# Kernel tuning notes

Measured on AMD Instinct MI355X. Metric: run time of the kernel, lower is better.

The kernel has to match this reference:

```python
import jax, jax.numpy as jnp
import numpy as np

DIM = 1024
HEADS = 16
SEQ_H = 32
SEQ_W = 32
HEAD_DIM = DIM // HEADS          # 64
ROT_DIM = HEAD_DIM // 4          # 16 per axis (lucidrains RotaryEmbedding dim)
FULL_ROT = 2 * ROT_DIM           # 32 channels rotated (axial: H-axis + W-axis)


def axial_freqs():
    # lucidrains 'pixel' mode: freqs = linspace(1, max_freq/2, dim//2) * pi, pos = linspace(-1, 1, steps)
    max_freq = SEQ_H * SEQ_W
    base = jnp.linspace(1.0, max_freq / 2.0, ROT_DIM // 2) * jnp.pi  # (rot//2,)
    th = jnp.linspace(-1.0, 1.0, SEQ_H)[:, None] * base[None, :]     # (H, rot//2)
    tw = jnp.linspace(-1.0, 1.0, SEQ_W)[:, None] * base[None, :]     # (W, rot//2)
    fh = jnp.repeat(th, 2, axis=-1)                                   # (H, rot)
    fw = jnpp_repeat = jnp.repeat(tw, 2, axis=-1)                     # (W, rot)
    fh = jnp.broadcast_to(fh[:, None, :], (SEQ_H, SEQ_W, ROT_DIM))
    fw = jnp.broadcast_to(fw[None, :, :], (SEQ_H, SEQ_W, ROT_DIM))
    return jnp.concatenate([fh, fw], axis=-1)                         # (H, W, FULL_ROT)


def rotate_half(t):
    # '... (d r) -> ... d r' with r=2, then (-x2, x1) interleaved back
    x = t.reshape(t.shape[:-1] + (t.shape[-1] // 2, 2))
    x1, x2 = x[..., 0], x[..., 1]
    return jnp.stack([-x2, x1], axis=-1).reshape(t.shape)


def apply_rope(t, cos, sin):
    # t: (B, heads, H, W, head_dim); only first FULL_ROT channels are rotated
    t_rot, t_pass = t[..., :FULL_ROT], t[..., FULL_ROT:]
    t_rot = t_rot * cos + rotate_half(t_rot) * sin
    return jnp.concatenate([t_rot, t_pass], axis=-1)


def setup_inputs() -> dict:
    key = jax.random.key(0)
    k1, k2, k3 = jax.random.split(key, 3)
    B, N = 8, SEQ_H * SEQ_W
    x = jax.random.normal(k1, (B, N, DIM), dtype=jnp.float32)
    Wqkv = jax.random.normal(k2, (3 * DIM, DIM), dtype=jnp.float32) * 0.02
    Wproj = jax.random.normal(k3, (DIM, DIM), dtype=jnp.float32) * 0.02
    bproj = jnp.zeros((DIM,), dtype=jnp.float32)
    return {"x": x, "Wqkv": Wqkv, "Wproj": Wproj, "bproj": bproj}


def reference(x, Wqkv, Wproj, bproj):
    B, N, C = x.shape
    qkv = jnp.einsum('bnc,fc->bnf', x, Wqkv)          # (B, N, 3C)
    q, k, v = jnp.split(qkv, 3, axis=-1)

    def to_grid(t):  # (B, N, C) -> (B, heads, H, W, hd)
        return t.reshape(B, SEQ_H, SEQ_W, HEADS, HEAD_DIM).transpose(0, 3, 1, 2, 4)

    q, k, v = to_grid(q), to_grid(k), to_grid(v)
    freqs = axial_freqs()
    cos, sin = jnp.cos(freqs), jnp.sin(freqs)         # (H, W, FULL_ROT)
    q = apply_rope(q, cos, sin)
    k = apply_rope(k, cos, sin)

    q = q.reshape(B, HEADS, N, HEAD_DIM)
    k = k.reshape(B, HEADS, N, HEAD_DIM)
    v = v.reshape(B, HEADS, N, HEAD_DIM)

    scale = 1.0 / jnp.sqrt(jnp.float32(HEAD_DIM))
    scores = jnp.einsum('bhqd,bhkd->bhqk', q, k) * scale
    attn = jax.nn.softmax(scores, axis=-1)
    out = jnp.einsum('bhqk,bhkd->bhqd', attn, v)       # (B, heads, N, hd)
    out = out.transpose(0, 2, 1, 3).reshape(B, N, C)
    return jnp.einsum('bnc,oc->bno', out, Wproj) + bproj
```

## Files before the change

### kernel.cpp

```cpp
#include <hip/hip_runtime.h>
#include <math.h>

#define DIM_ 1024
#define HEADS_ 16
#define HD_ 64
#define B_ 8
#define N_ 1024
#define M_TOT 8192

typedef __attribute__((ext_vector_type(4))) float f32x4;
typedef _Float16 v8h __attribute__((ext_vector_type(8)));
typedef __attribute__((ext_vector_type(4))) unsigned int u32x4;

static __device__ __forceinline__ unsigned short f2h(float x) {
  _Float16 h = (_Float16)x;
  return __builtin_bit_cast(unsigned short, h);
}
static __device__ __forceinline__ float fexp2(float x) {
  return __builtin_amdgcn_exp2f(x);
}
static __device__ __forceinline__ unsigned pkh2(float a, float b) {
  auto t = __builtin_amdgcn_cvt_pkrtz(a, b);
  return __builtin_bit_cast(unsigned, t);
}

static __device__ __forceinline__ void gload16(unsigned short* lds_base,
                                               const unsigned short* g) {
  __builtin_amdgcn_global_load_lds(
      (const __attribute__((address_space(1))) unsigned int*)g,
      (__attribute__((address_space(3))) unsigned int*)lds_base, 16, 0, 0);
}

__global__ __launch_bounds__(256) void split_all_k(
    const float* __restrict__ x, const float* __restrict__ wqkv,
    const float* __restrict__ wproj,
    unsigned short* __restrict__ xh, unsigned short* __restrict__ wqh,
    unsigned short* __restrict__ wph) {
  const int i = blockIdx.x * 256 + threadIdx.x;
  const float4* src;
  unsigned short* dst;
  int j;
  if (i < 2097152)      { j = i;           src = (const float4*)x;     dst = xh;  }
  else if (i < 2883584) { j = i - 2097152; src = (const float4*)wqkv;  dst = wqh; }
  else                  { j = i - 2883584; src = (const float4*)wproj; dst = wph; }
  float4 v = src[j];
  ushort4 h;
  h.x = f2h(v.x); h.y = f2h(v.y); h.z = f2h(v.z); h.w = f2h(v.w);
  ((ushort4*)dst)[j] = h;
}

__global__ void rope_table_k(float* cs, float* sn) {
  int i = threadIdx.x;
  if (i < 256) {
    int pos = i >> 3, j = i & 7;
    double u = -1.0 + (double)pos * (2.0/31.0);
    double ang = u * ((1.0 + 73.0*(double)j) * 3.14159265358979323846);
    cs[i] = (float)cos(ang);
    sn[i] = (float)sin(ang);
  }
}

static __device__ __forceinline__ void gemm_core1(
    const unsigned short* __restrict__ ah, const unsigned short* __restrict__ bh,
    unsigned short* S0, unsigned short* S2,
    int m0, int f0, f32x4 acc[4][4]) {
  const int tid = threadIdx.x;
  const int w = tid >> 6, l = tid & 63;
  const int lg = l >> 4, lc = l & 15;
  const int wr = w >> 1, wc = w & 1;
  const int r8 = l >> 3;
  const int ch = (l & 7) ^ r8;
  const int kc = ch * 8;
  for (int k0 = 0; k0 < 1024; k0 += 64) {
#pragma unroll
    for (int r = 0; r < 4; ++r) {
      const int row = r*32 + w*8 + r8;
      const size_t ao = (size_t)(m0 + row)*1024 + k0 + kc;
      const size_t bo = (size_t)(f0 + row)*1024 + k0 + kc;
      const int d = r*2048 + w*512;
      gload16(S0 + d, ah + ao);
      gload16(S2 + d, bh + bo);
    }
    __syncthreads();
#pragma unroll
    for (int c = 0; c < 2; ++c) {
      v8h a0[4], b0[4];
#pragma unroll
      for (int mi = 0; mi < 4; ++mi) {
        const int row = wr*64 + mi*16 + lc;
        const int bo = row*128 + ((c*64 + lg*16) ^ ((row & 7) << 4));
        a0[mi] = *(const v8h*)((const char*)S0 + bo);
      }
#pragma unroll
      for (int nj = 0; nj < 4; ++nj) {
        const int row = wc*64 + nj*16 + lc;
        const int bo = row*128 + ((c*64 + lg*16) ^ ((row & 7) << 4));
        b0[nj] = *(const v8h*)((const char*)S2 + bo);
      }
#pragma unroll
      for (int mi = 0; mi < 4; ++mi)
#pragma unroll
        for (int nj = 0; nj < 4; ++nj)
          acc[mi][nj] = __builtin_amdgcn_mfma_f32_16x16x32_f16(a0[mi], b0[nj], acc[mi][nj], 0, 0, 0);
    }
    __syncthreads();
  }
}

__global__ __launch_bounds__(256) void qk_gemm_mfma(
    const unsigned short* __restrict__ xh,
    const unsigned short* __restrict__ wh,
    const float* __restrict__ cs, const float* __restrict__ sn,
    unsigned short* __restrict__ qh, unsigned short* __restrict__ kh) {
  __shared__ unsigned short SM[16384];
  const int tid = threadIdx.x;
  const int w = tid >> 6, l = tid & 63;
  const int lg = l >> 4, lc = l & 15;
  const int wr = w >> 1, wc = w & 1;
  const int nwg = gridDim.x * gridDim.y;
  int bid = blockIdx.y * gridDim.x + blockIdx.x;
  bid = (bid & 7) * (nwg >> 3) + (bid >> 3);
  const int m0 = (bid / gridDim.x) * 128;
  const int f0 = (bid % gridDim.x) * 128;
  f32x4 acc[4][4] = {};
  gemm_core1(xh, wh, SM, SM + 8192, m0, f0, acc);
  const int qsel = f0 >> 10;
  const int head = ((f0 & 1023) >> 6) + wc;
  float* tbl = (float*)SM;
  tbl[tid] = cs[tid];
  tbl[256 + tid] = sn[tid];
  __syncthreads();
  const float scale = (qsel == 0) ? 0.18033688011112042f : 1.0f;
  unsigned short* oh = qsel ? kh : qh;
#pragma unroll
  for (int mi = 0; mi < 4; ++mi)
#pragma unroll
    for (int nj = 0; nj < 4; ++nj) {
      const int d = nj*16 + lc;
#pragma unroll
      for (int r = 0; r < 4; ++r) {
        const int m = m0 + wr*64 + mi*16 + lg*4 + r;
        const int b = m >> 10, n = m & 1023;
        float val = acc[mi][nj][r] * scale;
        float part = __shfl_xor(val, 1);
        if (nj < 2) {
          const int p = d >> 1;
          const int pos = (p < 8) ? (n >> 5) : (n & 31);
          const float c = tbl[pos*8 + (p & 7)];
          const float s = tbl[256 + pos*8 + (p & 7)];
          val = (d & 1) ? (val*c + part*s) : (val*c - part*s);
        }
        oh[((size_t)(b*HEADS_ + head)*N_ + n)*HD_ + d] = f2h(val);
      }
    }
}

__global__ __launch_bounds__(256) void v_gemm_mfma(
    const unsigned short* __restrict__ xh, const unsigned short* __restrict__ wh,
    unsigned short* __restrict__ vth) {
  __shared__ unsigned short SM[18432];
  const int tid = threadIdx.x;
  const int w = tid >> 6, l = tid & 63;
  const int lg = l >> 4, lc = l & 15;
  const int wr = w >> 1, wc = w & 1;
  const int nwg = gridDim.x * gridDim.y;
  int bid = blockIdx.y * gridDim.x + blockIdx.x;
  bid = (bid & 7) * (nwg >> 3) + (bid >> 3);
  const int m0 = (bid / gridDim.x) * 128;
  const int f0 = (bid % gridDim.x) * 128;
  f32x4 acc[4][4] = {};
  gemm_core1(xh, wh + (size_t)2048*1024, SM, SM + 8192, m0, f0, acc);
  __syncthreads();
  unsigned short* VT = SM + w * 4608;
#pragma unroll
  for (int mi = 0; mi < 4; ++mi)
#pragma unroll
    for (int nj = 0; nj < 4; ++nj)
#pragma unroll
      for (int r = 0; r < 4; r += 2) {
        const int ml = mi*16 + lg*4 + r;
        const int dl = nj*16 + lc;
        *(unsigned*)((char*)VT + dl*144 + ml*2) = pkh2(acc[mi][nj][r], acc[mi][nj][r+1]);
      }
  __syncthreads();
  const int b = m0 >> 10;
  const int n0 = (m0 & 1023) + wr*64;
  const int head = (f0 >> 6) + wc;
#pragma unroll
  for (int j = 0; j < 8; ++j) {
    const int dl = (l >> 3) + j*8;
    u32x4 val = *(const u32x4*)((const char*)VT + dl*144 + (l & 7)*16);
    *(u32x4*)(vth + ((size_t)((b*HEADS_ + head)*HD_ + dl))*N_ + n0 + (l & 7)*8) = val;
  }
}

__global__ __launch_bounds__(256) void proj_gemm_mfma(
    const unsigned short* __restrict__ ah,
    const unsigned short* __restrict__ wh,
    const float* __restrict__ bias, float* __restrict__ out) {
  __shared__ unsigned short SM[16384];
  const int tid = threadIdx.x;
  const int w = tid >> 6, l = tid & 63;
  const int lg = l >> 4, lc = l & 15;
  const int wr = w >> 1, wc = w & 1;
  const int nwg = gridDim.x * gridDim.y;
  int bid = blockIdx.y * gridDim.x + blockIdx.x;
  bid = (bid & 7) * (nwg >> 3) + (bid >> 3);
  const int m0 = (bid / gridDim.x) * 128;
  const int o0 = (bid % gridDim.x) * 128;
  f32x4 acc[4][4] = {};
  gemm_core1(ah, wh, SM, SM + 8192, m0, o0, acc);
#pragma unroll
  for (int nj = 0; nj < 4; ++nj) {
    const int o = o0 + wc*64 + nj*16 + lc;
    const float bv = bias[o];
#pragma unroll
    for (int mi = 0; mi < 4; ++mi)
#pragma unroll
      for (int r = 0; r < 4; ++r) {
        const int m = m0 + wr*64 + mi*16 + lg*4 + r;
        out[(size_t)m*DIM_ + o] = acc[mi][nj][r] + bv;
      }
  }
}

__global__ __launch_bounds__(256, 6) void attn_mfma_k(
    const unsigned short* __restrict__ qh,
    const unsigned short* __restrict__ kh,
    const unsigned short* __restrict__ vth,
    unsigned short* __restrict__ aoh) {
  __shared__ unsigned short KhS[4096];
  __shared__ unsigned short VhS[4096];
  __shared__ unsigned int Pws[4][512];
  const int tid = threadIdx.x;
  const int w = tid >> 6, l = tid & 63;
  const int lg = l >> 4, lc = l & 15;
  const int bh = blockIdx.x, qt = blockIdx.y;
  const size_t gb = (size_t)bh * (N_*HD_);

  v8h qf[2];
#pragma unroll
  for (int c = 0; c < 2; ++c)
    qf[c] = *(const v8h*)(qh + gb +
        (size_t)(qt*64 + w*16 + lc)*HD_ + c*32 + lg*8);
  f32x4 O[4];
#pragma unroll
  for (int dt = 0; dt < 4; ++dt) O[dt] = (f32x4){0.f, 0.f, 0.f, 0.f};
  float lrow = 0.f;

  const int sr8 = l >> 3;
  const int sch = (l & 7) ^ sr8;
  char* PB = (char*)&Pws[w][0];
  const int psw = (lc & 7) << 4;

  for (int t = 0; t < 16; ++t) {
#pragma unroll
    for (int i = 0; i < 2; ++i) {
      const int row = w*16 + i*8 + sr8;
      const int lb = (w*16 + i*8)*64;
      gload16(KhS + lb, kh + gb + (size_t)(t*64 + row)*HD_ + sch*8);
      gload16(VhS + lb, vth + gb + (size_t)row*N_ + t*64 + sch*8);
    }
    __syncthreads();
    f32x4 s[4];
    __builtin_amdgcn_s_setprio(1);
#pragma unroll
    for (int kt = 0; kt < 4; ++kt) {
      s[kt] = (f32x4){0.f, 0.f, 0.f, 0.f};
      const int row = kt*16 + lc;
      const int sw = (row & 7) << 4;
#pragma unroll
      for (int c = 0; c < 2; ++c) {
        v8h kf = *(const v8h*)((const char*)KhS + row*128 + ((c*64 + lg*16) ^ sw));
        s[kt] = __builtin_amdgcn_mfma_f32_16x16x32_f16(kf, qf[c], s[kt], 0, 0, 0);
      }
    }
    __builtin_amdgcn_s_setprio(0);
#pragma unroll
    for (int kt = 0; kt < 4; ++kt) {
      const float p0 = fexp2(s[kt][0]);
      const float p1 = fexp2(s[kt][1]);
      const float p2 = fexp2(s[kt][2]);
      const float p3 = fexp2(s[kt][3]);
      lrow += (p0 + p1) + (p2 + p3);
      uint2 pw;
      pw.x = pkh2(p0, p1);
      pw.y = pkh2(p2, p3);
      *(uint2*)(PB + lc*128 + ((kt*32 + lg*8) ^ psw)) = pw;
    }
    u32x4 pa[2];
#pragma unroll
    for (int c = 0; c < 2; ++c)
      pa[c] = *(const u32x4*)(PB + lc*128 + ((c*64 + lg*16) ^ psw));
    __builtin_amdgcn_s_setprio(1);
#pragma unroll
    for (int dt = 0; dt < 4; ++dt) {
      const int row = dt*16 + lc;
      const int sw = (row & 7) << 4;
#pragma unroll
      for (int c = 0; c < 2; ++c) {
        v8h vf = *(const v8h*)((const char*)VhS + row*128 + ((c*64 + lg*16) ^ sw));
        O[dt] = __builtin_amdgcn_mfma_f32_16x16x32_f16(
            __builtin_bit_cast(v8h, pa[c]), vf, O[dt], 0, 0, 0);
      }
    }
    __builtin_amdgcn_s_setprio(0);
    __syncthreads();
  }
  lrow += __shfl_xor(lrow, 16);
  lrow += __shfl_xor(lrow, 32);
  const int b = bh >> 4, h = bh & 15;
  const float myinv = 1.0f / lrow;
#pragma unroll
  for (int r = 0; r < 4; ++r) {
    const float iv = __shfl(myinv, lg*4 + r);
    const int n = qt*64 + w*16 + lg*4 + r;
    const size_t base = ((size_t)(b*N_ + n))*DIM_ + h*HD_ + lc;
#pragma unroll
    for (int dt = 0; dt < 4; ++dt)
      aoh[base + dt*16] = f2h(O[dt][r] * iv);
  }
}

extern "C" void kernel_launch(void* const* d_in, const int* in_sizes, int n_in,
                              void* d_out, int out_size, void* d_ws, size_t ws_size,
                              hipStream_t stream) {
  const float* x     = (const float*)d_in[0];
  const float* Wqkv  = (const float*)d_in[1];
  const float* Wproj = (const float*)d_in[2];
  const float* bproj = (const float*)d_in[3];
  float* out = (float*)d_out;

  unsigned short* xh  = (unsigned short*)d_ws;
  unsigned short* wqh = xh  + 8388608;
  unsigned short* wph = wqh + 3145728;
  unsigned short* qh  = wph + 1048576;
  unsigned short* kh  = qh  + 8388608;
  unsigned short* vth = kh  + 8388608;
  float* cs = (float*)(vth + 8388608);
  float* sn = cs + 256;
  unsigned short* aoh = xh;

  hipLaunchKernelGGL(rope_table_k, dim3(1), dim3(256), 0, stream, cs, sn);
  hipLaunchKernelGGL(split_all_k, dim3(12288), dim3(256), 0, stream,
                     x, Wqkv, Wproj, xh, wqh, wph);
  hipLaunchKernelGGL(qk_gemm_mfma, dim3(16, 64), dim3(256), 0, stream,
                     xh, wqh, cs, sn, qh, kh);
  hipLaunchKernelGGL(v_gemm_mfma, dim3(8, 64), dim3(256), 0, stream, xh, wqh, vth);
  hipLaunchKernelGGL(attn_mfma_k, dim3(128, 16), dim3(256), 0, stream,
                     qh, kh, vth, aoh);
  hipLaunchKernelGGL(proj_gemm_mfma, dim3(8, 64), dim3(256), 0, stream,
                     aoh, wph, bproj, out);
}
```

Baseline: 167.5 us.

## Permute K rows so P fragments stay in registers, dropping LDS round-trip

K rows are loaded into shared memory in a permuted order, so each lane's QK^T MFMA outputs already line up with the A-operand layout needed by the PV MFMA. The softmax probabilities can then be packed directly into registers, which removes the per-wave P shared-memory buffer and its write/read round-trip. With less LDS in use, the launch bound is raised to 8 waves per SIMD to allow higher occupancy. The key-order permutation must match exactly the row order of V along the key dimension, and the tighter register budget could cause spills.

```diff
diff --git a/kernel.cpp b/kernel.cpp
--- a/kernel.cpp
+++ b/kernel.cpp
@@ -224,14 +224,13 @@
   }
 }
 
-__global__ __launch_bounds__(256, 6) void attn_mfma_k(
+__global__ __launch_bounds__(256, 8) void attn_mfma_k(
     const unsigned short* __restrict__ qh,
     const unsigned short* __restrict__ kh,
     const unsigned short* __restrict__ vth,
     unsigned short* __restrict__ aoh) {
   __shared__ unsigned short KhS[4096];
   __shared__ unsigned short VhS[4096];
-  __shared__ unsigned int Pws[4][512];
   const int tid = threadIdx.x;
   const int w = tid >> 6, l = tid & 63;
   const int lg = l >> 4, lc = l & 15;
@@ -250,16 +249,14 @@
 
   const int sr8 = l >> 3;
   const int sch = (l & 7) ^ sr8;
-  char* PB = (char*)&Pws[w][0];
-  const int psw = (lc & 7) << 4;
+  const int sig0 = (w >> 1)*32 + (sr8 >> 2)*8 + (w & 1)*4 + (sr8 & 3);
 
   for (int t = 0; t < 16; ++t) {
 #pragma unroll
     for (int i = 0; i < 2; ++i) {
-      const int row = w*16 + i*8 + sr8;
       const int lb = (w*16 + i*8)*64;
-      gload16(KhS + lb, kh + gb + (size_t)(t*64 + row)*HD_ + sch*8);
-      gload16(VhS + lb, vth + gb + (size_t)row*N_ + t*64 + sch*8);
+      gload16(KhS + lb, kh + gb + (size_t)(t*64 + sig0 + i*16)*HD_ + sch*8);
+      gload16(VhS + lb, vth + gb + (size_t)(w*16 + i*8 + sr8)*N_ + t*64 + sch*8);
     }
     __syncthreads();
     f32x4 s[4];
@@ -276,22 +273,20 @@
       }
     }
     __builtin_amdgcn_s_setprio(0);
-#pragma unroll
-    for (int kt = 0; kt < 4; ++kt) {
-      const float p0 = fexp2(s[kt][0]);
-      const float p1 = fexp2(s[kt][1]);
-      const float p2 = fexp2(s[kt][2]);
-      const float p3 = fexp2(s[kt][3]);
-      lrow += (p0 + p1) + (p2 + p3);
-      uint2 pw;
-      pw.x = pkh2(p0, p1);
-      pw.y = pkh2(p2, p3);
-      *(uint2*)(PB + lc*128 + ((kt*32 + lg*8) ^ psw)) = pw;
-    }
     u32x4 pa[2];
 #pragma unroll
-    for (int c = 0; c < 2; ++c)
-      pa[c] = *(const u32x4*)(PB + lc*128 + ((c*64 + lg*16) ^ psw));
+    for (int c = 0; c < 2; ++c) {
+      const float p0 = fexp2(s[2*c][0]);
+      const float p1 = fexp2(s[2*c][1]);
+      const float p2 = fexp2(s[2*c][2]);
+      const float p3 = fexp2(s[2*c][3]);
+      const float p4 = fexp2(s[2*c+1][0]);
+      const float p5 = fexp2(s[2*c+1][1]);
+      const float p6 = fexp2(s[2*c+1][2]);
+      const float p7 = fexp2(s[2*c+1][3]);
+      lrow += ((p0 + p1) + (p2 + p3)) + ((p4 + p5) + (p6 + p7));
+      pa[c] = (u32x4){pkh2(p0, p1), pkh2(p2, p3), pkh2(p4, p5), pkh2(p6, p7)};
+    }
     __builtin_amdgcn_s_setprio(1);
 #pragma unroll
     for (int dt = 0; dt < 4; ++dt) {
```

Result: no change. 168.6 us (+0.7%).
